# Kernel optimization log

Hardware: AMD Instinct MI355X
Metric: run time of the kernel (lower is better)

Reference implementation:

```python
import jax, jax.numpy as jnp
import numpy as np

N_NODES = 10000
N_EDGES = 100000
D_IN = 2 * 1280   # concat of row/col node embeddings
H1 = 512
H2 = 256


def gcn_conv(x, edge_index, W, b):
    """PyG GCNConv: add self-loops, symmetric deg^-1/2 normalization,
    x @ W then scatter-add of normalized messages, plus bias.
    num_nodes is inferred from x.shape[0] (here = n_edges, faithful to source)."""
    N = x.shape[0]
    loops = jnp.arange(N, dtype=edge_index.dtype)
    row = jnp.concatenate([edge_index[0], loops])  # sources
    col = jnp.concatenate([edge_index[1], loops])  # targets
    deg = jax.ops.segment_sum(jnp.ones_like(row, dtype=x.dtype), col, num_segments=N)
    dinv = jax.lax.rsqrt(deg)  # deg >= 1 thanks to self-loops
    norm = dinv[row] * dinv[col]  # [E+N]
    h = x @ W  # [N, out]
    out = jax.ops.segment_sum(h[row] * norm[:, None], col, num_segments=N)
    return out + b


def setup_inputs() -> dict:
    key = jax.random.key(0)
    ks = jax.random.split(key, 9)
    x = jax.random.normal(ks[0], (N_NODES, 1280), dtype=jnp.float32)
    edge_index = jax.random.randint(ks[1], (2, N_EDGES), 0, N_NODES, dtype=jnp.int32)
    # uniform noise for gumbel-sigmoid (torch.rand); keep strictly in (0,1)
    eps = jax.random.uniform(ks[2], (N_EDGES, 1), jnp.float32, 1e-6, 1.0 - 1e-6)
    W1 = jax.random.normal(ks[3], (D_IN, H1), jnp.float32) * (1.0 / np.sqrt(D_IN))
    b1 = jnp.zeros((H1,), jnp.float32)
    W2 = jax.random.normal(ks[4], (H1, H2), jnp.float32) * (1.0 / np.sqrt(H1))
    b2 = jnp.zeros((H2,), jnp.float32)
    Wl = jax.random.normal(ks[5], (H2, 1), jnp.float32) * (1.0 / np.sqrt(H2))
    bl = jnp.zeros((1,), jnp.float32)
    return {"x": x, "edge_index": edge_index, "eps": eps,
            "W1": W1, "b1": b1, "W2": W2, "b2": b2, "Wl": Wl, "bl": bl}


def reference(x, edge_index, eps, W1, b1, W2, b2, Wl, bl):
    rows, cols = edge_index[0], edge_index[1]
    # per-edge explainer input: concat of endpoint embeddings -> [E, 2560]
    input_embs = jnp.concatenate([x[rows], x[cols]], axis=1)
    h = jax.nn.relu(gcn_conv(input_embs, edge_index, W1, b1))
    h = jax.nn.relu(gcn_conv(h, edge_index, W2, b2))
    pre = h @ Wl + bl  # [E, 1] sampling weights
    # gumbel-sigmoid sampling (temperature = 1.0)
    gate = jnp.log(eps) - jnp.log1p(-eps) + pre
    mask = jax.nn.sigmoid(gate)
    pos, neg = mask, 1.0 - mask
    kld = jnp.mean(pos * jnp.log(pos / 0.5 + 1e-8) + neg * jnp.log(neg / 0.5 + 1e-9))
    return (kld, mask)
```

## Files before the change

### kernel.cpp

```cpp
#include <hip/hip_runtime.h>
#include <cstdint>
#include <cstddef>

#define H1DIM 512
#define H2DIM 256
#define DNODE 1280
#define NPACK 1024
#define APAD  40

typedef __attribute__((ext_vector_type(8))) short short8v;
typedef __attribute__((ext_vector_type(4))) float f32x4;
typedef __attribute__((ext_vector_type(4))) unsigned short us4;

__device__ __forceinline__ unsigned short f2bf(float f) {
    unsigned int u = __builtin_bit_cast(unsigned int, f);
    u += 0x7fffu + ((u >> 16) & 1u);
    return (unsigned short)(u >> 16);
}
__device__ __forceinline__ float bf2f(unsigned short h) {
    unsigned int u = ((unsigned int)h) << 16;
    return __builtin_bit_cast(float, u);
}

__global__ void hist_k(const int* __restrict__ e1, int* __restrict__ hist, int E) {
    int e = blockIdx.x * 256 + threadIdx.x;
    if (e < E) atomicAdd(&hist[e1[e]], 1);
}
__global__ __launch_bounds__(1024) void scan_dinv_k(
    const int* __restrict__ hist, int* __restrict__ off, int* __restrict__ cursor,
    float* __restrict__ dinv, int N)
{
    __shared__ int part[1024];
    const int t = threadIdx.x;
    const int per = (N + 1023) / 1024;
    const int base = t * per;
    int s = 0;
    for (int i = 0; i < per; ++i) { int b = base + i; if (b < N) s += hist[b]; }
    part[t] = s;
    __syncthreads();
    for (int d = 1; d < 1024; d <<= 1) {
        int v = (t >= d) ? part[t - d] : 0;
        __syncthreads();
        part[t] += v;
        __syncthreads();
    }
    int run = (t == 0) ? 0 : part[t - 1];
    for (int i = 0; i < per; ++i) {
        int b = base + i;
        if (b < N) {
            int h = hist[b];
            off[b] = run;
            run += h;
            cursor[b] = 0;
            dinv[b] = rsqrtf(1.0f + (float)h);
        }
    }
    if (t == 1023) off[N] = run;
}
__global__ void fill_k(const int* __restrict__ e0, const int* __restrict__ e1,
                       const int* __restrict__ off, int* __restrict__ cursor,
                       int* __restrict__ srcs, int E) {
    int e = blockIdx.x * 256 + threadIdx.x;
    if (e < E) {
        int t = e1[e];
        int p = off[t] + atomicAdd(&cursor[t], 1);
        srcs[p] = e0[e];
    }
}

__global__ void cvt_x_k(const float* __restrict__ src, unsigned short* __restrict__ dst, int n) {
    int i = blockIdx.x * 256 + threadIdx.x;
    if (i * 4 < n) {
        f32x4 v = *reinterpret_cast<const f32x4*>(src + (size_t)i * 4);
        us4 o;
        o[0] = f2bf(v.x); o[1] = f2bf(v.y); o[2] = f2bf(v.z); o[3] = f2bf(v.w);
        *reinterpret_cast<us4*>(dst + (size_t)i * 4) = o;
    }
}

__global__ __launch_bounds__(256) void transpose_cvt_k(
    const float* __restrict__ src, unsigned short* __restrict__ dst, int ldsrc, int lddst)
{
    __shared__ float tile[32][33];
    const int c0 = blockIdx.x * 32;
    const int r0 = blockIdx.y * 32;
    const int tx = threadIdx.x & 31;
    const int ty = threadIdx.x >> 5;
#pragma unroll
    for (int rr = ty; rr < 32; rr += 8)
        tile[rr][tx] = src[(size_t)(r0 + rr) * ldsrc + c0 + tx];
    __syncthreads();
#pragma unroll
    for (int rr = ty; rr < 32; rr += 8)
        dst[(size_t)(c0 + rr) * lddst + r0 + tx] = f2bf(tile[tx][rr]);
}

template <int MODE>
__global__ __launch_bounds__(512) void gemm_u_k(
    const unsigned short* __restrict__ Ab,
    const unsigned short* __restrict__ Bt,
    unsigned short* __restrict__ Cb,
    const unsigned short* __restrict__ out1b,
    const unsigned short* __restrict__ XWb16,
    const float* __restrict__ b1,
    const float* __restrict__ b2,
    const float* __restrict__ Wl,
    const int* __restrict__ e0, const int* __restrict__ e1,
    unsigned short* __restrict__ h2b, float* __restrict__ pre_raw,
    int M, int K, int Nn, int nwg)
{
    __shared__ unsigned short As[2][128 * APAD];
    __shared__ unsigned short Bs[2][256 * APAD];
    __shared__ float b1s[H1DIM];
    __shared__ float b2s[H2DIM];
    __shared__ float wls[H2DIM];
    __shared__ float preacc[128];

    const int tid  = threadIdx.x;
    const int lane = tid & 63;
    const int w    = tid >> 6;
    const int wm   = w >> 2, wn = w & 3;

    int mb, n0;
    if (MODE == 0) {
        const int q = nwg >> 3, r = nwg & 7;
        const int xcd = blockIdx.x & 7;
        const int base = (xcd < r) ? xcd * (q + 1) : r * (q + 1) + (xcd - r) * q;
        const int wg = base + (blockIdx.x >> 3);
        mb = wg >> 2;
        n0 = (wg & 3) << 8;
    } else {
        mb = blockIdx.x;
        n0 = 0;
    }
    const int m0 = mb * 128;

    if (MODE == 1) {
        if (tid < 128) preacc[tid] = 0.f;
        if (tid < 256) { b2s[tid] = b2[tid]; wls[tid] = Wl[tid]; }
        b1s[tid] = b1[tid];
    }

    const int sa_r = tid >> 2, sa_k = (tid & 3) << 3;
    const int sb_r = tid >> 1, sb_k = (tid & 1) << 4;
    const int gma  = m0 + sa_r;
    const bool aval = (gma < M);

    const unsigned short* bsrc = Bt + (size_t)(n0 + sb_r) * K + sb_k;
    const unsigned short* s1 = nullptr;
    const unsigned short* s2 = nullptr;
    bool dual = false;
    if (MODE == 0) {
        if (aval) s1 = Ab + (size_t)gma * K + sa_k;
    } else if (aval) {
        if (gma < Nn) {
            s1 = out1b + (size_t)gma * H1DIM + sa_k;
        } else {
            s1 = XWb16 + (size_t)e0[gma] * NPACK + sa_k;
            s2 = XWb16 + (size_t)e1[gma] * NPACK + H1DIM + sa_k;
            dual = true;
        }
    }
    if (MODE == 1) __syncthreads();

    f32x4 acc[4][4];
#pragma unroll
    for (int i = 0; i < 4; ++i)
#pragma unroll
        for (int j = 0; j < 4; ++j) acc[i][j] = f32x4{0.f, 0.f, 0.f, 0.f};

    short8v ab1, ab2, bb0, bb1;

    auto load_tile = [&](int k0) {
        bb0 = *reinterpret_cast<const short8v*>(bsrc + k0);
        bb1 = *reinterpret_cast<const short8v*>(bsrc + k0 + 8);
        if (aval) {
            ab1 = *reinterpret_cast<const short8v*>(s1 + k0);
            if (MODE == 1 && dual) ab2 = *reinterpret_cast<const short8v*>(s2 + k0);
        }
    };
    auto write_lds = [&](int buf, int k0) {
        *reinterpret_cast<short8v*>(&Bs[buf][sb_r * APAD + sb_k])     = bb0;
        *reinterpret_cast<short8v*>(&Bs[buf][sb_r * APAD + sb_k + 8]) = bb1;
        short8v av;
        if (!aval) {
            av = short8v{0,0,0,0,0,0,0,0};
        } else if (MODE == 0 || !dual) {
            av = ab1;
        } else {
#pragma unroll
            for (int ii = 0; ii < 8; ++ii) {
                float v = bf2f((unsigned short)ab1[ii]) + bf2f((unsigned short)ab2[ii])
                        + b1s[k0 + sa_k + ii];
                v = fmaxf(v, 0.f);
                av[ii] = (short)f2bf(v);
            }
        }
        *reinterpret_cast<short8v*>(&As[buf][sa_r * APAD + sa_k]) = av;
    };

    const int arow = wm * 64 + (lane & 15);
    const int brow = wn * 64 + (lane & 15);
    const int kq   = (lane >> 4) << 3;

    load_tile(0);
    int buf = 0;
    for (int k0 = 0; k0 < K; k0 += 32) {
        write_lds(buf, k0);
        __syncthreads();
        if (k0 + 32 < K) load_tile(k0 + 32);

        const unsigned short* as = As[buf];
        const unsigned short* bs = Bs[buf];
        short8v af[4], bfq[4];
#pragma unroll
        for (int i = 0; i < 4; ++i)
            af[i] = *reinterpret_cast<const short8v*>(&as[(arow + i * 16) * APAD + kq]);
#pragma unroll
        for (int j = 0; j < 4; ++j)
            bfq[j] = *reinterpret_cast<const short8v*>(&bs[(brow + j * 16) * APAD + kq]);
#pragma unroll
        for (int i = 0; i < 4; ++i)
#pragma unroll
            for (int j = 0; j < 4; ++j)
                acc[i][j] = __builtin_amdgcn_mfma_f32_16x16x32_bf16(af[i], bfq[j], acc[i][j], 0, 0, 0);
        buf ^= 1;
    }

    const int crow0 = m0 + wm * 64 + ((lane >> 4) << 2);
    if (MODE == 0) {
        const int ccol = n0 + wn * 64 + (lane & 15);
#pragma unroll
        for (int i = 0; i < 4; ++i)
#pragma unroll
            for (int q = 0; q < 4; ++q) {
                const int row = crow0 + i * 16 + q;
                if (row < M) {
#pragma unroll
                    for (int j = 0; j < 4; ++j)
                        Cb[(size_t)row * NPACK + ccol + j * 16] = f2bf(acc[i][j][q]);
                }
            }
    } else {
        const int cbase = wn * 64 + (lane & 15);
#pragma unroll
        for (int i = 0; i < 4; ++i)
#pragma unroll
            for (int q = 0; q < 4; ++q) {
                float v = 0.f;
#pragma unroll
                for (int j = 0; j < 4; ++j) {
                    const int c = cbase + j * 16;
                    v += fmaxf(acc[i][j][q] + b2s[c], 0.f) * wls[c];
                }
                v += __shfl_xor(v, 1, 64);
                v += __shfl_xor(v, 2, 64);
                v += __shfl_xor(v, 4, 64);
                v += __shfl_xor(v, 8, 64);
                if ((lane & 15) == 0)
                    atomicAdd(&preacc[wm * 64 + i * 16 + ((lane >> 4) << 2) + q], v);
            }
        if (m0 < Nn) {
            const int ccol = wn * 64 + (lane & 15);
#pragma unroll
            for (int i = 0; i < 4; ++i)
#pragma unroll
                for (int q = 0; q < 4; ++q) {
                    const int row = crow0 + i * 16 + q;
                    if (row < Nn) {
#pragma unroll
                        for (int j = 0; j < 4; ++j)
                            h2b[(size_t)row * H2DIM + ccol + j * 16] = f2bf(acc[i][j][q]);
                    }
                }
        }
        __syncthreads();
        if (tid < 128) {
            const int gm = m0 + tid;
            if (gm >= Nn && gm < M) pre_raw[gm] = preacc[tid];
        }
    }
}

__global__ __launch_bounds__(256) void build1_k(
    const unsigned short* __restrict__ XWb16, const float* __restrict__ dinv,
    const int* __restrict__ e0, const int* __restrict__ e1,
    unsigned short* __restrict__ H1b)
{
    const int r = blockIdx.x;
    const int a = e0[r], b = e1[r];
    const float dv = dinv[r];
    const unsigned short* pt = XWb16 + (size_t)a * NPACK;
    const unsigned short* pb = XWb16 + (size_t)b * NPACK + H1DIM;
    const int j = threadIdx.x * 2;
    const unsigned ut = *reinterpret_cast<const unsigned*>(pt + j);
    const unsigned ub = *reinterpret_cast<const unsigned*>(pb + j);
    const float ox = (bf2f((unsigned short)(ut & 0xffff)) + bf2f((unsigned short)(ub & 0xffff))) * dv;
    const float oy = (bf2f((unsigned short)(ut >> 16))   + bf2f((unsigned short)(ub >> 16)))   * dv;
    const unsigned pk = (unsigned)f2bf(ox) | ((unsigned)f2bf(oy) << 16);
    *reinterpret_cast<unsigned*>(H1b + (size_t)r * H1DIM + j) = pk;
}

__global__ __launch_bounds__(256) void agg1_k(
    const unsigned short* __restrict__ H1b, const int* __restrict__ off, const int* __restrict__ srcs,
    const float* __restrict__ b1, const float* __restrict__ dinv,
    unsigned short* __restrict__ out1b)
{
    const int t = blockIdx.x;
    const int j = threadIdx.x * 2;
    const int s0 = off[t], s1e = off[t + 1];
    const float dt = dinv[t];
    const unsigned u0 = *reinterpret_cast<const unsigned*>(H1b + (size_t)t * H1DIM + j);
    float ax = bf2f((unsigned short)(u0 & 0xffff));
    float ay = bf2f((unsigned short)(u0 >> 16));
    for (int i = s0; i < s1e; ++i) {
        const unsigned v = *reinterpret_cast<const unsigned*>(H1b + (size_t)srcs[i] * H1DIM + j);
        ax += bf2f((unsigned short)(v & 0xffff));
        ay += bf2f((unsigned short)(v >> 16));
    }
    const float ox = fmaxf(b1[j]     + dt * ax, 0.f);
    const float oy = fmaxf(b1[j + 1] + dt * ay, 0.f);
    const unsigned pk = (unsigned)f2bf(ox) | ((unsigned)f2bf(oy) << 16);
    *reinterpret_cast<unsigned*>(out1b + (size_t)t * H1DIM + j) = pk;
}

__global__ __launch_bounds__(128) void agg2_k(
    const unsigned short* __restrict__ h2b, const int* __restrict__ off, const int* __restrict__ srcs,
    const float* __restrict__ b2, const float* __restrict__ Wl,
    const float* __restrict__ dinv, float* __restrict__ pre_low)
{
    __shared__ float part[2];
    const int t = blockIdx.x;
    const int j = threadIdx.x * 2;
    const int s0 = off[t], s1e = off[t + 1];
    const float dt = dinv[t];
    const unsigned u0 = *reinterpret_cast<const unsigned*>(h2b + (size_t)t * H2DIM + j);
    float ax = bf2f((unsigned short)(u0 & 0xffff)) * dt;
    float ay = bf2f((unsigned short)(u0 >> 16)) * dt;
    for (int i = s0; i < s1e; ++i) {
        const int s = srcs[i];
        const float ds = dinv[s];
        const unsigned v = *reinterpret_cast<const unsigned*>(h2b + (size_t)s * H2DIM + j);
        ax += bf2f((unsigned short)(v & 0xffff)) * ds;
        ay += bf2f((unsigned short)(v >> 16)) * ds;
    }
    float p = fmaxf(b2[j]     + dt * ax, 0.f) * Wl[j]
            + fmaxf(b2[j + 1] + dt * ay, 0.f) * Wl[j + 1];
#pragma unroll
    for (int o = 32; o; o >>= 1) p += __shfl_down(p, o, 64);
    if ((threadIdx.x & 63) == 0) part[threadIdx.x >> 6] = p;
    __syncthreads();
    if (threadIdx.x == 0) pre_low[t] = part[0] + part[1];
}

__global__ __launch_bounds__(256) void final2_k(
    const float* __restrict__ pre_low, const float* __restrict__ pre_raw,
    const float* __restrict__ blp, const float* __restrict__ eps,
    float* __restrict__ dout, int E, int Nn)
{
    __shared__ float part[4];
    const int i = blockIdx.x * 256 + threadIdx.x;
    float kld = 0.f;
    if (i < E) {
        const float pre = ((i < Nn) ? pre_low[i] : pre_raw[i]) + blp[0];
        const float ee = eps[i];
        const float gate = logf(ee) - log1pf(-ee) + pre;
        const float m = 1.0f / (1.0f + expf(-gate));
        dout[1 + i] = m;
        const float pos = m, neg = 1.0f - m;
        kld = pos * logf(pos * 2.0f + 1e-8f) + neg * logf(neg * 2.0f + 1e-9f);
    }
#pragma unroll
    for (int o = 32; o; o >>= 1) kld += __shfl_down(kld, o, 64);
    const int lane = threadIdx.x & 63, wv = threadIdx.x >> 6;
    if (lane == 0) part[wv] = kld;
    __syncthreads();
    if (threadIdx.x == 0)
        atomicAdd(&dout[0], (part[0] + part[1] + part[2] + part[3]) / (float)E);
}

extern "C" void kernel_launch(void* const* d_in, const int* in_sizes, int n_in,
                              void* d_out, int out_size, void* d_ws, size_t ws_size,
                              hipStream_t stream)
{
    const float* x   = (const float*)d_in[0];
    const int*   ei  = (const int*)d_in[1];
    const float* eps = (const float*)d_in[2];
    const float* W1  = (const float*)d_in[3];
    const float* b1  = (const float*)d_in[4];
    const float* W2  = (const float*)d_in[5];
    const float* b2  = (const float*)d_in[6];
    const float* Wl  = (const float*)d_in[7];
    const float* bl  = (const float*)d_in[8];
    float* out = (float*)d_out;
    float* ws  = (float*)d_ws;

    const int N = in_sizes[0] / DNODE;
    const int E = in_sizes[1] / 2;
    const int* e0 = ei;
    const int* e1 = ei + E;

    float* dinv     = ws;
    float* pre_raw  = dinv + 16384;
    float* pre_low  = pre_raw + E;
    float* fend     = pre_low + 16384;
    unsigned short* XWb16 = (unsigned short*)fend;
    unsigned short* out1b = XWb16 + (size_t)N * NPACK;
    unsigned short* H1b   = out1b + (size_t)N * H1DIM;
    unsigned short* h2b   = H1b + (size_t)N * H1DIM;
    unsigned short* xb    = h2b + (size_t)N * H2DIM;
    unsigned short* Bpt1  = xb + (size_t)N * DNODE;
    unsigned short* W2t   = Bpt1 + (size_t)NPACK * DNODE;
    int* hist   = (int*)(W2t + (size_t)H2DIM * H1DIM);
    int* cursor = hist + N;
    int* off    = cursor + N;
    int* srcs   = off + (N + 1);

    hipMemsetAsync(hist, 0, (size_t)N * sizeof(int), stream);
    hipMemsetAsync(out, 0, sizeof(float), stream);

    hist_k<<<(E + 255) / 256, 256, 0, stream>>>(e1, hist, E);
    scan_dinv_k<<<1, 1024, 0, stream>>>(hist, off, cursor, dinv, N);
    fill_k<<<(E + 255) / 256, 256, 0, stream>>>(e0, e1, off, cursor, srcs, E);

    cvt_x_k<<<(N * DNODE / 4 + 255) / 256, 256, 0, stream>>>(x, xb, N * DNODE);
    transpose_cvt_k<<<dim3(H1DIM / 32, DNODE / 32), 256, 0, stream>>>(W1, Bpt1, H1DIM, DNODE);
    transpose_cvt_k<<<dim3(H1DIM / 32, DNODE / 32), 256, 0, stream>>>(
        W1 + (size_t)DNODE * H1DIM, Bpt1 + (size_t)H1DIM * DNODE, H1DIM, DNODE);
    transpose_cvt_k<<<dim3(H2DIM / 32, H1DIM / 32), 256, 0, stream>>>(W2, W2t, H2DIM, H1DIM);

    {
        const int nwg = 4 * ((N + 127) / 128);
        gemm_u_k<0><<<nwg, 512, 0, stream>>>(
            xb, Bpt1, XWb16, nullptr, nullptr, b1, b2, Wl, e0, e1,
            nullptr, nullptr, N, DNODE, 0, nwg);
    }

    build1_k<<<N, 256, 0, stream>>>(XWb16, dinv, e0, e1, H1b);
    agg1_k<<<N, 256, 0, stream>>>(H1b, off, srcs, b1, dinv, out1b);

    {
        const int nwg = (E + 127) / 128;
        gemm_u_k<1><<<nwg, 512, 0, stream>>>(
            nullptr, W2t, nullptr, out1b, XWb16, b1, b2, Wl, e0, e1,
            h2b, pre_raw, E, H1DIM, N, nwg);
    }

    agg2_k<<<N, 128, 0, stream>>>(h2b, off, srcs, b2, Wl, dinv, pre_low);

    final2_k<<<(E + 255) / 256, 256, 0, stream>>>(pre_low, pre_raw, bl, eps, out, E, N);
}
```

Baseline: 218.8 us.

## Load GEMM tiles directly into LDS with global_load_lds in MFMA fragment order

```diff
diff --git a/kernel.cpp b/kernel.cpp
--- a/kernel.cpp
+++ b/kernel.cpp
@@ -6,7 +6,6 @@
 #define H2DIM 256
 #define DNODE 1280
 #define NPACK 1024
-#define APAD  40
 
 typedef __attribute__((ext_vector_type(8))) short short8v;
 typedef __attribute__((ext_vector_type(4))) float f32x4;
@@ -20,6 +19,13 @@
 __device__ __forceinline__ float bf2f(unsigned short h) {
     unsigned int u = ((unsigned int)h) << 16;
     return __builtin_bit_cast(float, u);
+}
+
+__device__ __forceinline__ void gload16(const unsigned short* g, unsigned short* l) {
+    __builtin_amdgcn_global_load_lds(
+        (const __attribute__((address_space(1))) void*)g,
+        (__attribute__((address_space(3))) void*)l,
+        16, 0, 0);
 }
 
 __global__ void hist_k(const int* __restrict__ e1, int* __restrict__ hist, int E) {
@@ -96,7 +102,7 @@
 }
 
 template <int MODE>
-__global__ __launch_bounds__(512) void gemm_u_k(
+__global__ __launch_bounds__(512, 4) void gemm_u_k(
     const unsigned short* __restrict__ Ab,
     const unsigned short* __restrict__ Bt,
     unsigned short* __restrict__ Cb,
@@ -109,8 +115,8 @@
     unsigned short* __restrict__ h2b, float* __restrict__ pre_raw,
     int M, int K, int Nn, int nwg)
 {
-    __shared__ unsigned short As[2][128 * APAD];
-    __shared__ unsigned short Bs[2][256 * APAD];
+    __shared__ alignas(16) unsigned short As[128 * 32];
+    __shared__ alignas(16) unsigned short Bs[256 * 32];
     __shared__ float b1s[H1DIM];
     __shared__ float b2s[H2DIM];
     __shared__ float wls[H2DIM];
@@ -139,29 +145,40 @@
         if (tid < 128) preacc[tid] = 0.f;
         if (tid < 256) { b2s[tid] = b2[tid]; wls[tid] = Wl[tid]; }
         b1s[tid] = b1[tid];
-    }
-
-    const int sa_r = tid >> 2, sa_k = (tid & 3) << 3;
-    const int sb_r = tid >> 1, sb_k = (tid & 1) << 4;
-    const int gma  = m0 + sa_r;
-    const bool aval = (gma < M);
-
-    const unsigned short* bsrc = Bt + (size_t)(n0 + sb_r) * K + sb_k;
+        __syncthreads();
+    }
+
+    const int brow_g = (lane & 15);
+    const int bcol_g = (lane >> 4) << 3;
+    const unsigned short* bs0 = Bt + (size_t)(n0 + (2 * w)     * 16 + brow_g) * K + bcol_g;
+    const unsigned short* bs1 = Bt + (size_t)(n0 + (2 * w + 1) * 16 + brow_g) * K + bcol_g;
+    unsigned short* bdst0 = &Bs[(2 * w)     * 512];
+    unsigned short* bdst1 = &Bs[(2 * w + 1) * 512];
+
+    const unsigned short* asrc = nullptr;
     const unsigned short* s1 = nullptr;
     const unsigned short* s2 = nullptr;
-    bool dual = false;
+    bool aval = true, dual = false;
+    int acol = 0;
     if (MODE == 0) {
-        if (aval) s1 = Ab + (size_t)gma * K + sa_k;
-    } else if (aval) {
-        if (gma < Nn) {
-            s1 = out1b + (size_t)gma * H1DIM + sa_k;
+        int ra = m0 + w * 16 + (lane & 15);
+        if (ra >= M) ra = M - 1;
+        asrc = Ab + (size_t)ra * K + bcol_g;
+    } else {
+        const int R   = ((tid >> 6) << 4) + (tid & 15);
+        const int gma = m0 + R;
+        const int gc  = (gma < M) ? gma : (M - 1);
+        acol = ((tid >> 4) & 3) << 3;
+        aval = (gma < M);
+        if (gc < Nn) {
+            s1 = out1b + (size_t)gc * H1DIM + acol;
+            s2 = s1;
         } else {
-            s1 = XWb16 + (size_t)e0[gma] * NPACK + sa_k;
-            s2 = XWb16 + (size_t)e1[gma] * NPACK + H1DIM + sa_k;
+            s1 = XWb16 + (size_t)e0[gc] * NPACK + acol;
+            s2 = XWb16 + (size_t)e1[gc] * NPACK + H1DIM + acol;
             dual = true;
         }
     }
-    if (MODE == 1) __syncthreads();
 
     f32x4 acc[4][4];
 #pragma unroll
@@ -169,62 +186,69 @@
 #pragma unroll
         for (int j = 0; j < 4; ++j) acc[i][j] = f32x4{0.f, 0.f, 0.f, 0.f};
 
-    short8v ab1, ab2, bb0, bb1;
-
-    auto load_tile = [&](int k0) {
-        bb0 = *reinterpret_cast<const short8v*>(bsrc + k0);
-        bb1 = *reinterpret_cast<const short8v*>(bsrc + k0 + 8);
-        if (aval) {
-            ab1 = *reinterpret_cast<const short8v*>(s1 + k0);
-            if (MODE == 1 && dual) ab2 = *reinterpret_cast<const short8v*>(s2 + k0);
+    const unsigned short* ard = &As[(wm * 4) * 512 + lane * 8];
+    const unsigned short* brd = &Bs[(wn * 4) * 512 + lane * 8];
+
+    short8v ab1, ab2;
+    if (MODE == 1) {
+        ab1 = *reinterpret_cast<const short8v*>(s1);
+        ab2 = *reinterpret_cast<const short8v*>(s2);
+    }
+
+    for (int k0 = 0; k0 < K; k0 += 32) {
+        if (MODE == 0) {
+            if (k0) __syncthreads();
+            gload16(asrc + k0, &As[w * 512]);
+            gload16(bs0 + k0, bdst0);
+            gload16(bs1 + k0, bdst1);
+            __syncthreads();
+        } else {
+            if (k0) {
+                __builtin_amdgcn_sched_barrier(0);
+                __builtin_amdgcn_s_barrier();
+                __builtin_amdgcn_sched_barrier(0);
+            }
+            short8v av;
+            if (!aval) {
+                av = short8v{0,0,0,0,0,0,0,0};
+            } else if (!dual) {
+                av = ab1;
+            } else {
+#pragma unroll
+                for (int ii = 0; ii < 8; ++ii) {
+                    float v = bf2f((unsigned short)ab1[ii]) + bf2f((unsigned short)ab2[ii])
+                            + b1s[k0 + acol + ii];
+                    v = fmaxf(v, 0.f);
+                    av[ii] = (short)f2bf(v);
+                }
+            }
+            *reinterpret_cast<short8v*>(&As[tid * 8]) = av;
+            gload16(bs0 + k0, bdst0);
+            gload16(bs1 + k0, bdst1);
+            __builtin_amdgcn_sched_barrier(0);
+            if (k0 + 32 < K) {
+                ab1 = *reinterpret_cast<const short8v*>(s1 + k0 + 32);
+                ab2 = *reinterpret_cast<const short8v*>(s2 + k0 + 32);
+                asm volatile("s_waitcnt vmcnt(2) lgkmcnt(0)" ::: "memory");
+            } else {
+                asm volatile("s_waitcnt vmcnt(0) lgkmcnt(0)" ::: "memory");
+            }
+            __builtin_amdgcn_s_barrier();
+            __builtin_amdgcn_sched_barrier(0);
         }
-    };
-    auto write_lds = [&](int buf, int k0) {
-        *reinterpret_cast<short8v*>(&Bs[buf][sb_r * APAD + sb_k])     = bb0;
-        *reinterpret_cast<short8v*>(&Bs[buf][sb_r * APAD + sb_k + 8]) = bb1;
-        short8v av;
-        if (!aval) {
-            av = short8v{0,0,0,0,0,0,0,0};
-        } else if (MODE == 0 || !dual) {
-            av = ab1;
-        } else {
-#pragma unroll
-            for (int ii = 0; ii < 8; ++ii) {
-                float v = bf2f((unsigned short)ab1[ii]) + bf2f((unsigned short)ab2[ii])
-                        + b1s[k0 + sa_k + ii];
-                v = fmaxf(v, 0.f);
-                av[ii] = (short)f2bf(v);
-            }
-        }
-        *reinterpret_cast<short8v*>(&As[buf][sa_r * APAD + sa_k]) = av;
-    };
-
-    const int arow = wm * 64 + (lane & 15);
-    const int brow = wn * 64 + (lane & 15);
-    const int kq   = (lane >> 4) << 3;
-
-    load_tile(0);
-    int buf = 0;
-    for (int k0 = 0; k0 < K; k0 += 32) {
-        write_lds(buf, k0);
-        __syncthreads();
-        if (k0 + 32 < K) load_tile(k0 + 32);
-
-        const unsigned short* as = As[buf];
-        const unsigned short* bs = Bs[buf];
+
         short8v af[4], bfq[4];
 #pragma unroll
         for (int i = 0; i < 4; ++i)
-            af[i] = *reinterpret_cast<const short8v*>(&as[(arow + i * 16) * APAD + kq]);
+            af[i] = *reinterpret_cast<const short8v*>(ard + i * 512);
 #pragma unroll
         for (int j = 0; j < 4; ++j)
-            bfq[j] = *reinterpret_cast<const short8v*>(&bs[(brow + j * 16) * APAD + kq]);
+            bfq[j] = *reinterpret_cast<const short8v*>(brd + j * 512);
 #pragma unroll
         for (int i = 0; i < 4; ++i)
 #pragma unroll
             for (int j = 0; j < 4; ++j)
                 acc[i][j] = __builtin_amdgcn_mfma_f32_16x16x32_bf16(af[i], bfq[j], acc[i][j], 0, 0, 0);
-        buf ^= 1;
     }
 
     const int crow0 = m0 + wm * 64 + ((lane >> 4) << 2);
```

Measured after the change: 251.0 us. 14.8% more time.
